# Optimization experiments

Measured on AMD Instinct MI355X. Metric: run time of the kernel, lower is better.

## Reference

```python
import jax, jax.numpy as jnp
import numpy as np

N = 131072      # octree nodes at this depth
C_IN = 256      # in_channels == out_channels
C_B = 64        # bottleneck channels = out_channels // 4
K = 27          # 3x3x3 octree kernel neighborhood
EPS = 1e-5


def _bn(x, g, b, m, v):
    # inference-style BatchNorm with given running stats
    return (x - m) * (g * jax.lax.rsqrt(v + EPS)) + b


def setup_inputs() -> dict:
    key = jax.random.key(0)
    ks = jax.random.split(key, 20)
    inp = {
        "data": jax.random.normal(ks[0], (N, C_IN), dtype=jnp.float32),
        "neigh": jax.random.randint(ks[1], (N, K), 0, N, dtype=jnp.int32),
        "depth": 6,
        # conv1x1a (Linear, no bias) + BN
        "w1": jax.random.normal(ks[2], (C_IN, C_B), dtype=jnp.float32) * 0.05,
        "bn1_g": jax.random.uniform(ks[3], (C_B,), dtype=jnp.float32) + 0.5,
        "bn1_b": jax.random.normal(ks[4], (C_B,), dtype=jnp.float32) * 0.1,
        "bn1_m": jax.random.normal(ks[5], (C_B,), dtype=jnp.float32) * 0.1,
        "bn1_v": jax.random.uniform(ks[6], (C_B,), dtype=jnp.float32) + 0.5,
        # octree conv3x3 (27-neighbor gather + GEMM, no bias) + BN
        "w3": jax.random.normal(ks[7], (K, C_B, C_B), dtype=jnp.float32) * 0.02,
        "bn2_g": jax.random.uniform(ks[8], (C_B,), dtype=jnp.float32) + 0.5,
        "bn2_b": jax.random.normal(ks[9], (C_B,), dtype=jnp.float32) * 0.1,
        "bn2_m": jax.random.normal(ks[10], (C_B,), dtype=jnp.float32) * 0.1,
        "bn2_v": jax.random.uniform(ks[11], (C_B,), dtype=jnp.float32) + 0.5,
        # conv1x1b + BN (no ReLU)
        "w2": jax.random.normal(ks[12], (C_B, C_IN), dtype=jnp.float32) * 0.05,
        "bn3_g": jax.random.uniform(ks[13], (C_IN,), dtype=jnp.float32) + 0.5,
        "bn3_b": jax.random.normal(ks[14], (C_IN,), dtype=jnp.float32) * 0.1,
        "bn3_m": jax.random.normal(ks[15], (C_IN,), dtype=jnp.float32) * 0.1,
        "bn3_v": jax.random.uniform(ks[16], (C_IN,), dtype=jnp.float32) + 0.5,
    }
    return inp


def reference(data, neigh, depth, w1, bn1_g, bn1_b, bn1_m, bn1_v,
              w3, bn2_g, bn2_b, bn2_m, bn2_v,
              w2, bn3_g, bn3_b, bn3_m, bn3_v):
    # conv1x1a + BN + ReLU
    c1 = jax.nn.relu(_bn(data @ w1, bn1_g, bn1_b, bn1_m, bn1_v))  # [N, C_B]
    # octree conv3x3: gather 27 neighbors then contract with [K, C_B, C_B]
    gathered = c1[neigh]                                          # [N, K, C_B]
    c2 = jnp.einsum('nkc,kcd->nd', gathered, w3)                  # [N, C_B]
    c2 = jax.nn.relu(_bn(c2, bn2_g, bn2_b, bn2_m, bn2_v))
    # conv1x1b + BN (no relu)
    c3 = _bn(c2 @ w2, bn3_g, bn3_b, bn3_m, bn3_v)                 # [N, C_IN]
    # residual (in_channels == out_channels -> identity shortcut) + ReLU
    return jax.nn.relu(c3 + data)
```

## Files before the change

### kernel.cpp

```cpp
#include <hip/hip_runtime.h>

#define NN 131072
#define CIN 256
#define CB 64
#define KNB 27

typedef __attribute__((ext_vector_type(8))) short short8_t;
typedef __attribute__((ext_vector_type(4))) float f32x4;

__device__ inline unsigned short f2bf(float f) {
    union { float f; unsigned u; } x; x.f = f;
    unsigned r = x.u + 0x7fffu + ((x.u >> 16) & 1u);
    return (unsigned short)(r >> 16);
}

__device__ inline f32x4 mfma16(short8_t a, short8_t b, f32x4 c) {
    return __builtin_amdgcn_mfma_f32_16x16x32_bf16(a, b, c, 0, 0, 0);
}

__global__ __launch_bounds__(256) void prep_kernel(
    const float* __restrict__ w1, const float* __restrict__ w3, const float* __restrict__ w2,
    const float* __restrict__ g1, const float* __restrict__ b1, const float* __restrict__ m1, const float* __restrict__ v1,
    const float* __restrict__ g2, const float* __restrict__ b2, const float* __restrict__ m2, const float* __restrict__ v2,
    const float* __restrict__ g3, const float* __restrict__ b3, const float* __restrict__ m3, const float* __restrict__ v3,
    unsigned short* __restrict__ w1p, unsigned short* __restrict__ w3p, unsigned short* __restrict__ w2p,
    float* __restrict__ bias1, float* __restrict__ bias2, float* __restrict__ bias3)
{
    int t = blockIdx.x * 256 + threadIdx.x;
    if (t < 16384) {
        int j = t & 7, lane = (t >> 3) & 63, tt = (t >> 9) & 3, s = t >> 11;
        int c = s * 32 + (lane >> 4) * 8 + j;
        int d = tt * 16 + (lane & 15);
        float sc = g1[d] * rsqrtf(v1[d] + 1e-5f);
        w1p[t] = f2bf(w1[c * CB + d] * sc);
    } else if (t < 16384 + 110592) {
        int u = t - 16384;
        int j = u & 7, lane = (u >> 3) & 63, tt = (u >> 9) & 3, s = (u >> 11) & 1, k = u >> 12;
        int c = s * 32 + (lane >> 4) * 8 + j;
        int d = tt * 16 + (lane & 15);
        float sc = g2[d] * rsqrtf(v2[d] + 1e-5f);
        w3p[u] = f2bf(w3[(k * CB + c) * CB + d] * sc);
    } else if (t < 143360) {
        int u = t - 126976;
        int j = u & 7, lane = (u >> 3) & 63, ct = (u >> 9) & 15, s = u >> 13;
        int c = s * 32 + (lane >> 4) * 8 + j;
        int d = ct * 16 + (lane & 15);
        float sc = g3[d] * rsqrtf(v3[d] + 1e-5f);
        w2p[u] = f2bf(w2[c * CIN + d] * sc);
    } else if (t < 143744) {
        int u = t - 143360;
        if (u < 64)       { float sc = g1[u] * rsqrtf(v1[u] + 1e-5f); bias1[u] = b1[u] - m1[u] * sc; }
        else if (u < 128) { int d = u - 64;  float sc = g2[d] * rsqrtf(v2[d] + 1e-5f); bias2[d] = b2[d] - m2[d] * sc; }
        else              { int d = u - 128; float sc = g3[d] * rsqrtf(v3[d] + 1e-5f); bias3[d] = b3[d] - m3[d] * sc; }
    }
}

__global__ __launch_bounds__(256) void k1_conv1x1a(
    const float* __restrict__ data, const unsigned short* __restrict__ w1p,
    const float* __restrict__ bias1, unsigned short* __restrict__ c1b)
{
    __shared__ short8_t w1s[2048];
    int tid = threadIdx.x;
    const short8_t* wsrc = (const short8_t*)w1p;
#pragma unroll
    for (int i = 0; i < 8; i++) w1s[tid + i * 256] = wsrc[tid + i * 256];

    int lane = tid & 63, wave = tid >> 6;
    int g = lane >> 4, r = lane & 15;
    int rowbase = blockIdx.x * 128 + wave * 32;
    f32x4 acc[2][4] = {};
    __syncthreads();

#pragma unroll
    for (int s = 0; s < 8; s++) {
        short8_t a[2];
#pragma unroll
        for (int sub = 0; sub < 2; sub++) {
            const float* ap = data + (size_t)(rowbase + sub * 16 + r) * CIN + s * 32 + g * 8;
            float4 f0 = *(const float4*)ap;
            float4 f1 = *(const float4*)(ap + 4);
            short8_t av;
            av[0] = (short)f2bf(f0.x); av[1] = (short)f2bf(f0.y);
            av[2] = (short)f2bf(f0.z); av[3] = (short)f2bf(f0.w);
            av[4] = (short)f2bf(f1.x); av[5] = (short)f2bf(f1.y);
            av[6] = (short)f2bf(f1.z); av[7] = (short)f2bf(f1.w);
            a[sub] = av;
        }
#pragma unroll
        for (int t = 0; t < 4; t++) {
            short8_t b = w1s[(s * 4 + t) * 64 + lane];
            acc[0][t] = mfma16(a[0], b, acc[0][t]);
            acc[1][t] = mfma16(a[1], b, acc[1][t]);
        }
    }

#pragma unroll
    for (int sub = 0; sub < 2; sub++)
#pragma unroll
        for (int t = 0; t < 4; t++) {
            int col = t * 16 + r;
            float bs = bias1[col];
#pragma unroll
            for (int i = 0; i < 4; i++) {
                int row = rowbase + sub * 16 + g * 4 + i;
                c1b[row * CB + col] = f2bf(fmaxf(acc[sub][t][i] + bs, 0.f));
            }
        }
}

#define K2_MFMA(aX, bX) \
    _Pragma("unroll") for (int t = 0; t < 4; t++) { \
        acc[0][t] = mfma16(aX[0], bX[t],     acc[0][t]); \
        acc[1][t] = mfma16(aX[2], bX[t],     acc[1][t]); \
        acc[0][t] = mfma16(aX[1], bX[4 + t], acc[0][t]); \
        acc[1][t] = mfma16(aX[3], bX[4 + t], acc[1][t]); \
    }

#define K2_BODY(aC, bC, ixC0, ixC1, aN, bN, ixN0, ixN1, k) \
    { \
        if ((k) < 26) { \
            const short8_t* p0 = (const short8_t*)(c1b + (size_t)(ixN0) * CB); \
            const short8_t* p1 = (const short8_t*)(c1b + (size_t)(ixN1) * CB); \
            aN[0] = p0[g]; aN[1] = p0[4 + g]; aN[2] = p1[g]; aN[3] = p1[4 + g]; \
            const short8_t* bp = bbase + ((k) + 1) * 512; \
            _Pragma("unroll") for (int f = 0; f < 8; f++) bN[f] = bp[f * 64 + lane]; \
        } \
        if ((k) < 25) { ixC0 = nidx[lr0 * KNB + (k) + 2]; ixC1 = nidx[lr1 * KNB + (k) + 2]; } \
        K2_MFMA(aC, bC) \
    }

__global__ __launch_bounds__(256, 3) void k2_conv3x3(
    const unsigned short* __restrict__ c1b, const int* __restrict__ neigh,
    const unsigned short* __restrict__ w3p, const float* __restrict__ bias2,
    unsigned short* __restrict__ c2b)
{
    __shared__ int nidx[128 * KNB];
    int tid = threadIdx.x;
    int rowbase = blockIdx.x * 128;

    const int4* nsrc = (const int4*)(neigh + (size_t)rowbase * KNB);
#pragma unroll
    for (int i = 0; i < 4; i++) {
        int p = tid + i * 256;
        if (p < 864) ((int4*)nidx)[p] = nsrc[p];
    }

    int lane = tid & 63, wave = tid >> 6;
    int g = lane >> 4, r = lane & 15;
    int lr0 = wave * 32 + r, lr1 = lr0 + 16;
    __syncthreads();

    const short8_t* bbase = (const short8_t*)w3p;
    f32x4 acc[2][4] = {};
    short8_t aA[4], aB[4], bA[8], bB[8];
    int ixA0, ixA1, ixB0, ixB1;

    ixA0 = nidx[lr0 * KNB + 0]; ixA1 = nidx[lr1 * KNB + 0];
    ixB0 = nidx[lr0 * KNB + 1]; ixB1 = nidx[lr1 * KNB + 1];
    {
        const short8_t* p0 = (const short8_t*)(c1b + (size_t)ixA0 * CB);
        const short8_t* p1 = (const short8_t*)(c1b + (size_t)ixA1 * CB);
        aA[0] = p0[g]; aA[1] = p0[4 + g]; aA[2] = p1[g]; aA[3] = p1[4 + g];
#pragma unroll
        for (int f = 0; f < 8; f++) bA[f] = bbase[f * 64 + lane];
    }

    for (int kk = 0; kk < 13; kk++) {
        int k0 = kk * 2;
        K2_BODY(aA, bA, ixA0, ixA1, aB, bB, ixB0, ixB1, k0)
        K2_BODY(aB, bB, ixB0, ixB1, aA, bA, ixA0, ixA1, k0 + 1)
    }
    K2_BODY(aA, bA, ixA0, ixA1, aB, bB, ixB0, ixB1, 26)

#pragma unroll
    for (int sub = 0; sub < 2; sub++)
#pragma unroll
        for (int t = 0; t < 4; t++) {
            int col = t * 16 + r;
            float bs = bias2[col];
#pragma unroll
            for (int i = 0; i < 4; i++) {
                int row = rowbase + wave * 32 + sub * 16 + g * 4 + i;
                c2b[row * CB + col] = f2bf(fmaxf(acc[sub][t][i] + bs, 0.f));
            }
        }
}

__global__ __launch_bounds__(256) void k3_conv1x1b(
    const unsigned short* __restrict__ c2b, const unsigned short* __restrict__ w2p,
    const float* __restrict__ bias3, const float* __restrict__ data,
    float* __restrict__ out)
{
    __shared__ float otile[64 * 260];
    int tid = threadIdx.x;
    int lane = tid & 63, wave = tid >> 6;
    int g = lane >> 4, r = lane & 15;
    int rowbase = blockIdx.x * 64;

    const short8_t* bbase = (const short8_t*)w2p;
    short8_t a[4][2];
#pragma unroll
    for (int sub = 0; sub < 4; sub++) {
        const short8_t* ap = (const short8_t*)(c2b + (size_t)(rowbase + sub * 16 + r) * CB);
        a[sub][0] = ap[g];
        a[sub][1] = ap[4 + g];
    }
    f32x4 acc[4][4] = {};
#pragma unroll
    for (int s = 0; s < 2; s++)
#pragma unroll
        for (int t = 0; t < 4; t++) {
            short8_t b = bbase[(s * 16 + wave * 4 + t) * 64 + lane];
#pragma unroll
            for (int sub = 0; sub < 4; sub++)
                acc[sub][t] = mfma16(a[sub][s], b, acc[sub][t]);
        }

#pragma unroll
    for (int sub = 0; sub < 4; sub++)
#pragma unroll
        for (int t = 0; t < 4; t++) {
            int col = (wave * 4 + t) * 16 + r;
            float bs = bias3[col];
#pragma unroll
            for (int i = 0; i < 4; i++) {
                int row = sub * 16 + g * 4 + i;
                otile[row * 260 + col] = acc[sub][t][i] + bs;
            }
        }
    __syncthreads();

    const float* dsrc = data + (size_t)rowbase * CIN;
    float* dst = out + (size_t)rowbase * CIN;
#pragma unroll
    for (int p = 0; p < 16; p++) {
        int flat = p * 1024 + tid * 4;
        int row = flat >> 8, col = flat & 255;
        float4 dv = *(const float4*)(dsrc + flat);
        float4 ov = *(const float4*)(&otile[row * 260 + col]);
        float4 res;
        res.x = fmaxf(ov.x + dv.x, 0.f);
        res.y = fmaxf(ov.y + dv.y, 0.f);
        res.z = fmaxf(ov.z + dv.z, 0.f);
        res.w = fmaxf(ov.w + dv.w, 0.f);
        *(float4*)(dst + flat) = res;
    }
}

extern "C" void kernel_launch(void* const* d_in, const int* in_sizes, int n_in,
                              void* d_out, int out_size, void* d_ws, size_t ws_size,
                              hipStream_t stream)
{
    const float* data = (const float*)d_in[0];
    const int* neigh  = (const int*)d_in[1];
    const float* w1 = (const float*)d_in[3];
    const float* g1 = (const float*)d_in[4];
    const float* b1 = (const float*)d_in[5];
    const float* m1 = (const float*)d_in[6];
    const float* v1 = (const float*)d_in[7];
    const float* w3 = (const float*)d_in[8];
    const float* g2 = (const float*)d_in[9];
    const float* b2 = (const float*)d_in[10];
    const float* v2 = (const float*)d_in[12];
    const float* m2 = (const float*)d_in[11];
    const float* w2 = (const float*)d_in[13];
    const float* g3 = (const float*)d_in[14];
    const float* b3 = (const float*)d_in[15];
    const float* m3 = (const float*)d_in[16];
    const float* v3 = (const float*)d_in[17];
    float* out = (float*)d_out;

    char* ws = (char*)d_ws;
    unsigned short* c1b = (unsigned short*)ws;
    unsigned short* c2b = (unsigned short*)(ws + 16777216);
    unsigned short* w1p = (unsigned short*)(ws + 33554432);
    unsigned short* w3p = (unsigned short*)(ws + 33554432 + 32768);
    unsigned short* w2p = (unsigned short*)(ws + 33554432 + 32768 + 221184);
    float* bias1 = (float*)(ws + 33554432 + 32768 + 221184 + 32768);
    float* bias2 = bias1 + 64;
    float* bias3 = bias1 + 128;

    int n = in_sizes[0] / CIN;

    hipLaunchKernelGGL(prep_kernel, dim3(562), dim3(256), 0, stream,
                       w1, w3, w2, g1, b1, m1, v1, g2, b2, m2, v2, g3, b3, m3, v3,
                       w1p, w3p, w2p, bias1, bias2, bias3);
    hipLaunchKernelGGL(k1_conv1x1a, dim3(n / 128), dim3(256), 0, stream, data, w1p, bias1, c1b);
    hipLaunchKernelGGL(k2_conv3x3,  dim3(n / 128), dim3(256), 0, stream, c1b, neigh, w3p, bias2, c2b);
    hipLaunchKernelGGL(k3_conv1x1b, dim3(n / 64),  dim3(256), 0, stream, c2b, w2p, bias3, data, out);
}
```

Measured before the change: 172.5 us.

## Fuse octree conv3x3 with conv1x1b and residual epilogue into one kernel

Merges the 27-neighbor conv kernel with the second 1x1 conv plus residual kernel. The bf16 c2 tile is staged in shared memory, reusing the neighbor-index buffer, instead of making a global round trip, and the final GEMM is computed in transposed form (w2 as the A operand) so each lane writes float4 output directly. The w3 weight fragments are no longer double-buffered in registers; they are loaded just before use, to cut register pressure, and the launch_bounds occupancy hint is dropped. This saves a kernel launch and the c2 write and read, at the risk of exposing weight-load latency and of less coalesced output and data accesses.

Measured after the change: 202.7 us. +17.5%, slower.

```diff
diff --git a/kernel.cpp b/kernel.cpp
--- a/kernel.cpp
+++ b/kernel.cpp
@@ -42,9 +42,9 @@
         w3p[u] = f2bf(w3[(k * CB + c) * CB + d] * sc);
     } else if (t < 143360) {
         int u = t - 126976;
-        int j = u & 7, lane = (u >> 3) & 63, ct = (u >> 9) & 15, s = u >> 13;
+        int j = u & 7, lane = (u >> 3) & 63, mt = (u >> 9) & 15, s = u >> 13;
         int c = s * 32 + (lane >> 4) * 8 + j;
-        int d = ct * 16 + (lane & 15);
+        int d = mt * 16 + (lane & 15);
         float sc = g3[d] * rsqrtf(v3[d] + 1e-5f);
         w2p[u] = f2bf(w2[c * CIN + d] * sc);
     } else if (t < 143744) {
@@ -116,25 +116,28 @@
         acc[1][t] = mfma16(aX[3], bX[4 + t], acc[1][t]); \
     }
 
-#define K2_BODY(aC, bC, ixC0, ixC1, aN, bN, ixN0, ixN1, k) \
+#define K23_STEP(aC, aN, ixC0, ixC1, ixN0, ixN1, k) \
     { \
+        short8_t bl[8]; \
+        const short8_t* bp = bbase + (size_t)(k) * 512; \
+        _Pragma("unroll") for (int f = 0; f < 8; f++) bl[f] = bp[f * 64 + lane]; \
         if ((k) < 26) { \
             const short8_t* p0 = (const short8_t*)(c1b + (size_t)(ixN0) * CB); \
             const short8_t* p1 = (const short8_t*)(c1b + (size_t)(ixN1) * CB); \
             aN[0] = p0[g]; aN[1] = p0[4 + g]; aN[2] = p1[g]; aN[3] = p1[4 + g]; \
-            const short8_t* bp = bbase + ((k) + 1) * 512; \
-            _Pragma("unroll") for (int f = 0; f < 8; f++) bN[f] = bp[f * 64 + lane]; \
         } \
         if ((k) < 25) { ixC0 = nidx[lr0 * KNB + (k) + 2]; ixC1 = nidx[lr1 * KNB + (k) + 2]; } \
-        K2_MFMA(aC, bC) \
-    }
-
-__global__ __launch_bounds__(256, 3) void k2_conv3x3(
+        K2_MFMA(aC, bl) \
+    }
+
+__global__ __launch_bounds__(256) void k23_fused(
     const unsigned short* __restrict__ c1b, const int* __restrict__ neigh,
     const unsigned short* __restrict__ w3p, const float* __restrict__ bias2,
-    unsigned short* __restrict__ c2b)
-{
-    __shared__ int nidx[128 * KNB];
+    const unsigned short* __restrict__ w2p, const float* __restrict__ bias3,
+    const float* __restrict__ data, float* __restrict__ out)
+{
+    __shared__ __align__(16) char shraw[17408];
+    int* nidx = (int*)shraw;
     int tid = threadIdx.x;
     int rowbase = blockIdx.x * 128;
 
@@ -152,7 +155,7 @@
 
     const short8_t* bbase = (const short8_t*)w3p;
     f32x4 acc[2][4] = {};
-    short8_t aA[4], aB[4], bA[8], bB[8];
+    short8_t aA[4], aB[4];
     int ixA0, ixA1, ixB0, ixB1;
 
     ixA0 = nidx[lr0 * KNB + 0]; ixA1 = nidx[lr1 * KNB + 0];
@@ -161,17 +164,17 @@
         const short8_t* p0 = (const short8_t*)(c1b + (size_t)ixA0 * CB);
         const short8_t* p1 = (const short8_t*)(c1b + (size_t)ixA1 * CB);
         aA[0] = p0[g]; aA[1] = p0[4 + g]; aA[2] = p1[g]; aA[3] = p1[4 + g];
-#pragma unroll
-        for (int f = 0; f < 8; f++) bA[f] = bbase[f * 64 + lane];
     }
 
     for (int kk = 0; kk < 13; kk++) {
         int k0 = kk * 2;
-        K2_BODY(aA, bA, ixA0, ixA1, aB, bB, ixB0, ixB1, k0)
-        K2_BODY(aB, bB, ixB0, ixB1, aA, bA, ixA0, ixA1, k0 + 1)
-    }
-    K2_BODY(aA, bA, ixA0, ixA1, aB, bB, ixB0, ixB1, 26)
-
+        K23_STEP(aA, aB, ixA0, ixA1, ixB0, ixB1, k0)
+        K23_STEP(aB, aA, ixB0, ixB1, ixA0, ixA1, k0 + 1)
+    }
+    K23_STEP(aA, aB, ixA0, ixA1, ixB0, ixB1, 26)
+
+    __syncthreads();
+    unsigned short* cst = (unsigned short*)shraw + wave * 2176;
 #pragma unroll
     for (int sub = 0; sub < 2; sub++)
 #pragma unroll
@@ -180,70 +183,48 @@
             float bs = bias2[col];
 #pragma unroll
             for (int i = 0; i < 4; i++) {
-                int row = rowbase + wave * 32 + sub * 16 + g * 4 + i;
-                c2b[row * CB + col] = f2bf(fmaxf(acc[sub][t][i] + bs, 0.f));
+                int row = sub * 16 + g * 4 + i;
+                cst[row * 68 + col] = f2bf(fmaxf(acc[sub][t][i] + bs, 0.f));
             }
         }
-}
-
-__global__ __launch_bounds__(256) void k3_conv1x1b(
-    const unsigned short* __restrict__ c2b, const unsigned short* __restrict__ w2p,
-    const float* __restrict__ bias3, const float* __restrict__ data,
-    float* __restrict__ out)
-{
-    __shared__ float otile[64 * 260];
-    int tid = threadIdx.x;
-    int lane = tid & 63, wave = tid >> 6;
-    int g = lane >> 4, r = lane & 15;
-    int rowbase = blockIdx.x * 64;
-
-    const short8_t* bbase = (const short8_t*)w2p;
-    short8_t a[4][2];
-#pragma unroll
-    for (int sub = 0; sub < 4; sub++) {
-        const short8_t* ap = (const short8_t*)(c2b + (size_t)(rowbase + sub * 16 + r) * CB);
-        a[sub][0] = ap[g];
-        a[sub][1] = ap[4 + g];
-    }
-    f32x4 acc[4][4] = {};
-#pragma unroll
-    for (int s = 0; s < 2; s++)
-#pragma unroll
-        for (int t = 0; t < 4; t++) {
-            short8_t b = bbase[(s * 16 + wave * 4 + t) * 64 + lane];
-#pragma unroll
-            for (int sub = 0; sub < 4; sub++)
-                acc[sub][t] = mfma16(a[sub][s], b, acc[sub][t]);
-        }
-
-#pragma unroll
-    for (int sub = 0; sub < 4; sub++)
-#pragma unroll
-        for (int t = 0; t < 4; t++) {
-            int col = (wave * 4 + t) * 16 + r;
-            float bs = bias3[col];
-#pragma unroll
-            for (int i = 0; i < 4; i++) {
-                int row = sub * 16 + g * 4 + i;
-                otile[row * 260 + col] = acc[sub][t][i] + bs;
+    __syncthreads();
+
+    short8_t bfr[2][2];
+#pragma unroll
+    for (int sub = 0; sub < 2; sub++)
+#pragma unroll
+        for (int s = 0; s < 2; s++)
+            bfr[sub][s] = *(const short8_t*)(cst + (sub * 16 + r) * 68 + s * 32 + g * 8);
+
+    const short8_t* abase = (const short8_t*)w2p;
+#pragma unroll
+    for (int h = 0; h < 2; h++) {
+        f32x4 acc2[2][8] = {};
+#pragma unroll
+        for (int mt = 0; mt < 8; mt++) {
+            short8_t a0 = abase[(h * 8 + mt) * 64 + lane];
+            short8_t a1 = abase[(16 + h * 8 + mt) * 64 + lane];
+            acc2[0][mt] = mfma16(a0, bfr[0][0], acc2[0][mt]);
+            acc2[0][mt] = mfma16(a1, bfr[0][1], acc2[0][mt]);
+            acc2[1][mt] = mfma16(a0, bfr[1][0], acc2[1][mt]);
+            acc2[1][mt] = mfma16(a1, bfr[1][1], acc2[1][mt]);
+        }
+#pragma unroll
+        for (int sub = 0; sub < 2; sub++)
+#pragma unroll
+            for (int mt = 0; mt < 8; mt++) {
+                int col0 = (h * 8 + mt) * 16 + g * 4;
+                int rowg = rowbase + wave * 32 + sub * 16 + r;
+                float4 bs = *(const float4*)(bias3 + col0);
+                float4 dv = *(const float4*)(data + (size_t)rowg * CIN + col0);
+                f32x4 v = acc2[sub][mt];
+                float4 res;
+                res.x = fmaxf(v[0] + bs.x + dv.x, 0.f);
+                res.y = fmaxf(v[1] + bs.y + dv.y, 0.f);
+                res.z = fmaxf(v[2] + bs.z + dv.z, 0.f);
+                res.w = fmaxf(v[3] + bs.w + dv.w, 0.f);
+                *(float4*)(out + (size_t)rowg * CIN + col0) = res;
             }
-        }
-    __syncthreads();
-
-    const float* dsrc = data + (size_t)rowbase * CIN;
-    float* dst = out + (size_t)rowbase * CIN;
-#pragma unroll
-    for (int p = 0; p < 16; p++) {
-        int flat = p * 1024 + tid * 4;
-        int row = flat >> 8, col = flat & 255;
-        float4 dv = *(const float4*)(dsrc + flat);
-        float4 ov = *(const float4*)(&otile[row * 260 + col]);
-        float4 res;
-        res.x = fmaxf(ov.x + dv.x, 0.f);
-        res.y = fmaxf(ov.y + dv.y, 0.f);
-        res.z = fmaxf(ov.z + dv.z, 0.f);
-        res.w = fmaxf(ov.w + dv.w, 0.f);
-        *(float4*)(dst + flat) = res;
     }
 }
 
@@ -261,8 +242,8 @@
     const float* w3 = (const float*)d_in[8];
     const float* g2 = (const float*)d_in[9];
     const float* b2 = (const float*)d_in[10];
+    const float* m2 = (const float*)d_in[11];
     const float* v2 = (const float*)d_in[12];
-    const float* m2 = (const float*)d_in[11];
     const float* w2 = (const float*)d_in[13];
     const float* g3 = (const float*)d_in[14];
     const float* b3 = (const float*)d_in[15];
@@ -272,7 +253,6 @@
 
     char* ws = (char*)d_ws;
     unsigned short* c1b = (unsigned short*)ws;
-    unsigned short* c2b = (unsigned short*)(ws + 16777216);
     unsigned short* w1p = (unsigned short*)(ws + 33554432);
     unsigned short* w3p = (unsigned short*)(ws + 33554432 + 32768);
     unsigned short* w2p = (unsigned short*)(ws + 33554432 + 32768 + 221184);
@@ -286,6 +266,6 @@
                        w1, w3, w2, g1, b1, m1, v1, g2, b2, m2, v2, g3, b3, m3, v3,
                        w1p, w3p, w2p, bias1, bias2, bias3);
     hipLaunchKernelGGL(k1_conv1x1a, dim3(n / 128), dim3(256), 0, stream, data, w1p, bias1, c1b);
-    hipLaunchKernelGGL(k2_conv3x3,  dim3(n / 128), dim3(256), 0, stream, c1b, neigh, w3p, bias2, c2b);
-    hipLaunchKernelGGL(k3_conv1x1b, dim3(n / 64),  dim3(256), 0, stream, c2b, w2p, bias3, data, out);
-}
+    hipLaunchKernelGGL(k23_fused,   dim3(n / 128), dim3(256), 0, stream,
+                       c1b, neigh, w3p, bias2, w2p, bias3, data, out);
+}
```
